# Optimization experiments

Measured on AMD Instinct MI355X. Metric: run time of the kernel, lower is better.

## Reference

```python
import jax, jax.numpy as jnp
import numpy as np

N = 100000       # nodes
E = 1600000      # edges (avg degree 16)
D_IN = 256
D_HID = 64
D_OUT = 40
PROP_STEP = 16
ALP = 0.5
LAM = 1.0


def setup_inputs() -> dict:
    key = jax.random.key(0)
    ks = jax.random.split(key, 9)
    x = jax.random.normal(ks[0], (N, D_IN), dtype=jnp.float32)
    edge_row = jnp.sort(jax.random.randint(ks[1], (E,), 0, N, dtype=jnp.int32))
    edge_col = jax.random.randint(ks[2], (E,), 0, N, dtype=jnp.int32)
    # normalized-adjacency-like nonnegative values, scaled ~1/deg for stability
    edge_val = jax.random.uniform(ks[3], (E,), dtype=jnp.float32) * (1.0 / 16.0)
    diag_vals = jax.random.uniform(ks[4], (N,), dtype=jnp.float32)
    # MLP params (xavier-normal-ish init, zero bias)
    W1 = jax.random.normal(ks[5], (D_IN, D_HID), dtype=jnp.float32) * np.sqrt(2.0 / (D_IN + D_HID))
    b1 = jnp.zeros((D_HID,), dtype=jnp.float32)
    W2 = jax.random.normal(ks[6], (D_HID, D_OUT), dtype=jnp.float32) * np.sqrt(2.0 / (D_HID + D_OUT))
    b2 = jnp.zeros((D_OUT,), dtype=jnp.float32)
    return {"x": x, "edge_row": edge_row, "edge_col": edge_col,
            "edge_val": edge_val, "diag_vals": diag_vals,
            "W1": W1, "b1": b1, "W2": W2, "b2": b2}


def _spmm(edge_row, edge_col, edge_val, Y):
    # sparse [N,N] @ dense [N,D] via gather + segment-sum
    msgs = edge_val[:, None] * Y[edge_col]          # [E, D]
    return jax.ops.segment_sum(msgs, edge_row, num_segments=N)


def reference(x, edge_row, edge_col, edge_val, diag_vals, W1, b1, W2, b2):
    # mlp_bef: single Linear (num_mlp_before=1, no activation after last layer)
    h = x @ W1 + b1                                  # [N, D_HID]
    # spmm(norm_diag, h) is loop-invariant: norm_diag is diagonal
    src = ALP * diag_vals[:, None] * h               # [N, D_HID]
    Y = h
    for _ in range(PROP_STEP):
        Y = (1.0 - ALP) * Y + (ALP * LAM) * _spmm(edge_row, edge_col, edge_val, Y) + src
    # mlp_aft: init_activate=True -> ReLU (norm='none', dropout=0), then Linear
    Y = jax.nn.relu(Y)
    return Y @ W2 + b2                               # [N, D_OUT]
```

## Files before the change

### kernel.cpp

```cpp
#include <hip/hip_runtime.h>

#define N_NODES 100000
#define N_EDGES 1600000
#define D_IN    256
#define D_HID   64
#define D_OUT   40
#define PROP_N  16

typedef short short8 __attribute__((ext_vector_type(8)));
typedef float f32x4  __attribute__((ext_vector_type(4)));

__device__ __forceinline__ unsigned char f32_to_fp8(float f) {
    int p = __builtin_amdgcn_cvt_pk_fp8_f32(f, f, 0, false);
    return (unsigned char)(p & 0xff);
}
__device__ __forceinline__ unsigned short f32_to_bf16(float f) {
    unsigned int u = __float_as_uint(f);
    unsigned int r = (u + 0x7fffu + ((u >> 16) & 1u)) >> 16;
    return (unsigned short)r;
}
__device__ __forceinline__ unsigned int f32x2_to_bf16x2(float lo, float hi) {
    return (unsigned int)f32_to_bf16(lo) | ((unsigned int)f32_to_bf16(hi) << 16);
}
__device__ __forceinline__ float bf16_f(unsigned short u) {
    return __uint_as_float(((unsigned)u) << 16);
}
__device__ __forceinline__ float edge_val(unsigned p) {
    return __uint_as_float((p & 0x7fffu) << 16);
}
__device__ __forceinline__ void fma4(float4& a, float v, unsigned b) {
    a.x = fmaf(v, __builtin_amdgcn_cvt_f32_fp8((int)b, 0), a.x);
    a.y = fmaf(v, __builtin_amdgcn_cvt_f32_fp8((int)b, 1), a.y);
    a.z = fmaf(v, __builtin_amdgcn_cvt_f32_fp8((int)b, 2), a.z);
    a.w = fmaf(v, __builtin_amdgcn_cvt_f32_fp8((int)b, 3), a.w);
}

__global__ __launch_bounds__(256) void build_rowptr(const int* __restrict__ erow,
                                                    int* __restrict__ rp) {
    int r = blockIdx.x * blockDim.x + threadIdx.x;
    if (r > N_NODES) return;
    int lo = 0, hi = N_EDGES;
    while (lo < hi) {
        int mid = (lo + hi) >> 1;
        if (erow[mid] < r) lo = mid + 1; else hi = mid;
    }
    rp[r] = lo;
}

__global__ __launch_bounds__(256) void pack_edges4(const int* __restrict__ ecol,
                                                   const float* __restrict__ evalv,
                                                   unsigned* __restrict__ ep4) {
    int i = blockIdx.x * blockDim.x + threadIdx.x;
    if (i >= N_EDGES) return;
    unsigned bf = f32_to_bf16(evalv[i]);
    ep4[i] = ((unsigned)ecol[i] << 15) | (bf & 0x7fffu);
}

__global__ __launch_bounds__(256) void prep_w1t(const float* __restrict__ W1,
                                                unsigned short* __restrict__ W1T) {
    int i = blockIdx.x * 256 + threadIdx.x;
    if (i >= D_IN * D_HID) return;
    int k = i >> 6, n = i & 63;
    W1T[n * 256 + k] = f32_to_bf16(W1[i]);
}

__global__ __launch_bounds__(64) void mlp1(const float* __restrict__ x,
                                           const unsigned short* __restrict__ W1T,
                                           const float* __restrict__ b1,
                                           const float* __restrict__ diag,
                                           unsigned short* __restrict__ Yb,
                                           unsigned char* __restrict__ Y08,
                                           unsigned short* __restrict__ srcb) {
    const int lane  = threadIdx.x;
    const int l15   = lane & 15;
    const int quad  = lane >> 4;
    const int mbase = blockIdx.x * 16;

    f32x4 acc[4] = {};
    const float* xrow = x + (size_t)(mbase + l15) * D_IN + quad * 8;

    #pragma unroll
    for (int ks = 0; ks < 8; ++ks) {
        float4 f0 = *(const float4*)(xrow + ks * 32);
        float4 f1 = *(const float4*)(xrow + ks * 32 + 4);
        union { short8 v; unsigned int u[4]; } a;
        a.u[0] = f32x2_to_bf16x2(f0.x, f0.y);
        a.u[1] = f32x2_to_bf16x2(f0.z, f0.w);
        a.u[2] = f32x2_to_bf16x2(f1.x, f1.y);
        a.u[3] = f32x2_to_bf16x2(f1.z, f1.w);

        #pragma unroll
        for (int ct = 0; ct < 4; ++ct) {
            short8 b = *(const short8*)(W1T + (ct * 16 + l15) * 256 + ks * 32 + quad * 8);
            acc[ct] = __builtin_amdgcn_mfma_f32_16x16x32_bf16(a.v, b, acc[ct], 0, 0, 0);
        }
    }

    float bias[4];
    #pragma unroll
    for (int ct = 0; ct < 4; ++ct) bias[ct] = b1[ct * 16 + l15];

    #pragma unroll
    for (int reg = 0; reg < 4; ++reg) {
        const int mr = mbase + quad * 4 + reg;
        const float dg = diag[mr];
        #pragma unroll
        for (int ct = 0; ct < 4; ++ct) {
            const int col = ct * 16 + l15;
            const float h = acc[ct][reg] + bias[ct];
            const size_t idx = (size_t)mr * 64 + col;
            Yb[idx]   = f32_to_bf16(h);
            srcb[idx] = f32_to_bf16(0.5f * dg * h);
            Y08[idx]  = f32_to_fp8(h);
        }
    }
}

__global__ __launch_bounds__(256) void prop_step(const unsigned short* __restrict__ Yb,
                                                 const unsigned char* __restrict__ Y8,
                                                 const unsigned short* __restrict__ srcb,
                                                 unsigned short* __restrict__ Ybo,
                                                 unsigned char* __restrict__ Yo8,
                                                 const int* __restrict__ rp,
                                                 const unsigned* __restrict__ ep4) {
    const int wid  = blockIdx.x * 4 + (threadIdx.x >> 6);
    const int lane = threadIdx.x & 63;
    const int g    = lane >> 4;
    const int fl   = lane & 15;
    const int row  = wid * 4 + g;

    const int e0 = rp[row];
    const int e1 = rp[row + 1];

    const size_t fb = (size_t)row * 64 + fl * 4;
    const ushort4 ys4 = *(const ushort4*)(Yb + fb);
    const ushort4 sv4 = *(const ushort4*)(srcb + fb);
    const float4 yself = make_float4(bf16_f(ys4.x), bf16_f(ys4.y),
                                     bf16_f(ys4.z), bf16_f(ys4.w));
    const float4 sv    = make_float4(bf16_f(sv4.x), bf16_f(sv4.y),
                                     bf16_f(sv4.z), bf16_f(sv4.w));
    const unsigned char* Y8f = Y8 + fl * 4;

    float4 acc0 = make_float4(0.f, 0.f, 0.f, 0.f);
    float4 acc1 = acc0, acc2 = acc0, acc3 = acc0;

    int e = e0;
    int ea = (e0 + 3) & ~3;
    if (ea > e1) ea = e1;
    for (; e < ea; ++e) {
        unsigned p = ep4[e];
        unsigned b = *(const unsigned*)(Y8f + ((size_t)(p >> 15) << 6));
        fma4(acc0, edge_val(p), b);
    }
    for (; e + 8 <= e1; e += 8) {
        uint4 pa = *(const uint4*)(ep4 + e);
        uint4 pb = *(const uint4*)(ep4 + e + 4);
        unsigned b0 = *(const unsigned*)(Y8f + ((size_t)(pa.x >> 15) << 6));
        unsigned b1 = *(const unsigned*)(Y8f + ((size_t)(pa.y >> 15) << 6));
        unsigned b2 = *(const unsigned*)(Y8f + ((size_t)(pa.z >> 15) << 6));
        unsigned b3 = *(const unsigned*)(Y8f + ((size_t)(pa.w >> 15) << 6));
        unsigned b4 = *(const unsigned*)(Y8f + ((size_t)(pb.x >> 15) << 6));
        unsigned b5 = *(const unsigned*)(Y8f + ((size_t)(pb.y >> 15) << 6));
        unsigned b6 = *(const unsigned*)(Y8f + ((size_t)(pb.z >> 15) << 6));
        unsigned b7 = *(const unsigned*)(Y8f + ((size_t)(pb.w >> 15) << 6));
        fma4(acc0, edge_val(pa.x), b0);
        fma4(acc1, edge_val(pa.y), b1);
        fma4(acc2, edge_val(pa.z), b2);
        fma4(acc3, edge_val(pa.w), b3);
        fma4(acc0, edge_val(pb.x), b4);
        fma4(acc1, edge_val(pb.y), b5);
        fma4(acc2, edge_val(pb.z), b6);
        fma4(acc3, edge_val(pb.w), b7);
    }
    if (e + 4 <= e1) {
        uint4 pa = *(const uint4*)(ep4 + e);
        unsigned b0 = *(const unsigned*)(Y8f + ((size_t)(pa.x >> 15) << 6));
        unsigned b1 = *(const unsigned*)(Y8f + ((size_t)(pa.y >> 15) << 6));
        unsigned b2 = *(const unsigned*)(Y8f + ((size_t)(pa.z >> 15) << 6));
        unsigned b3 = *(const unsigned*)(Y8f + ((size_t)(pa.w >> 15) << 6));
        fma4(acc0, edge_val(pa.x), b0);
        fma4(acc1, edge_val(pa.y), b1);
        fma4(acc2, edge_val(pa.z), b2);
        fma4(acc3, edge_val(pa.w), b3);
        e += 4;
    }
    for (; e < e1; ++e) {
        unsigned p = ep4[e];
        unsigned b = *(const unsigned*)(Y8f + ((size_t)(p >> 15) << 6));
        fma4(acc0, edge_val(p), b);
    }

    float4 accs;
    accs.x = (acc0.x + acc1.x) + (acc2.x + acc3.x);
    accs.y = (acc0.y + acc1.y) + (acc2.y + acc3.y);
    accs.z = (acc0.z + acc1.z) + (acc2.z + acc3.z);
    accs.w = (acc0.w + acc1.w) + (acc2.w + acc3.w);

    float4 o;
    o.x = fmaf(0.5f, yself.x, fmaf(0.5f, accs.x, sv.x));
    o.y = fmaf(0.5f, yself.y, fmaf(0.5f, accs.y, sv.y));
    o.z = fmaf(0.5f, yself.z, fmaf(0.5f, accs.z, sv.z));
    o.w = fmaf(0.5f, yself.w, fmaf(0.5f, accs.w, sv.w));

    ushort4 ob;
    ob.x = f32_to_bf16(o.x); ob.y = f32_to_bf16(o.y);
    ob.z = f32_to_bf16(o.z); ob.w = f32_to_bf16(o.w);
    *(ushort4*)(Ybo + fb) = ob;
    int pk = __builtin_amdgcn_cvt_pk_fp8_f32(o.x, o.y, 0, false);
    pk     = __builtin_amdgcn_cvt_pk_fp8_f32(o.z, o.w, pk, true);
    *(unsigned*)(Yo8 + fb) = (unsigned)pk;
}

__global__ __launch_bounds__(256) void mlp2(const unsigned short* __restrict__ Yb,
                                            const float* __restrict__ W2,
                                            const float* __restrict__ b2,
                                            float* __restrict__ out) {
    __shared__ float W2s[D_HID * D_OUT];
    __shared__ float b2s[D_OUT];
    int tid = threadIdx.x;
    for (int i = tid; i < D_HID * D_OUT; i += 256) W2s[i] = W2[i];
    if (tid < D_OUT) b2s[tid] = b2[tid];
    __syncthreads();

    int n = blockIdx.x * 256 + tid;
    if (n >= N_NODES) return;

    float acc[D_OUT];
    #pragma unroll
    for (int o = 0; o < D_OUT; ++o) acc[o] = b2s[o];

    const uint4* Y4 = (const uint4*)(Yb + (size_t)n * 64);
    #pragma unroll
    for (int k8 = 0; k8 < 8; ++k8) {
        uint4 y = Y4[k8];
        unsigned w[4] = {y.x, y.y, y.z, y.w};
        #pragma unroll
        for (int d = 0; d < 4; ++d) {
            float lo = fmaxf(__uint_as_float((w[d] & 0xffffu) << 16), 0.0f);
            float hi = fmaxf(__uint_as_float(w[d] & 0xffff0000u), 0.0f);
            int klo = k8 * 8 + 2 * d, khi = klo + 1;
            #pragma unroll
            for (int o = 0; o < D_OUT; ++o)
                acc[o] = fmaf(lo, W2s[klo * D_OUT + o], acc[o]);
            #pragma unroll
            for (int o = 0; o < D_OUT; ++o)
                acc[o] = fmaf(hi, W2s[khi * D_OUT + o], acc[o]);
        }
    }

    float4* o4 = (float4*)(out + (size_t)n * D_OUT);
    #pragma unroll
    for (int q = 0; q < 10; ++q)
        o4[q] = make_float4(acc[4 * q], acc[4 * q + 1], acc[4 * q + 2], acc[4 * q + 3]);
}

extern "C" void kernel_launch(void* const* d_in, const int* in_sizes, int n_in,
                              void* d_out, int out_size, void* d_ws, size_t ws_size,
                              hipStream_t stream) {
    const float* x     = (const float*)d_in[0];
    const int*   erow  = (const int*)  d_in[1];
    const int*   ecol  = (const int*)  d_in[2];
    const float* evalv = (const float*)d_in[3];
    const float* diag  = (const float*)d_in[4];
    const float* W1    = (const float*)d_in[5];
    const float* b1    = (const float*)d_in[6];
    const float* W2    = (const float*)d_in[7];
    const float* b2    = (const float*)d_in[8];
    float* out = (float*)d_out;

    const size_t NV = (size_t)N_NODES * D_HID;
    unsigned short* Yb0  = (unsigned short*)d_ws;
    unsigned short* Yb1  = Yb0 + NV;
    unsigned short* srcb = Yb1 + NV;
    unsigned char*  Y08  = (unsigned char*)(srcb + NV);
    unsigned char*  Y18  = Y08 + NV;
    unsigned*       ep4  = (unsigned*)(Y18 + NV);
    int*            rp   = (int*)(ep4 + N_EDGES);
    unsigned short* W1T  = (unsigned short*)
        (((unsigned long long)(rp + N_NODES + 1) + 15ull) & ~15ull);

    build_rowptr<<<(N_NODES + 1 + 255) / 256, 256, 0, stream>>>(erow, rp);
    pack_edges4<<<(N_EDGES + 255) / 256, 256, 0, stream>>>(ecol, evalv, ep4);
    prep_w1t<<<(D_IN * D_HID + 255) / 256, 256, 0, stream>>>(W1, W1T);
    mlp1<<<N_NODES / 16, 64, 0, stream>>>(x, W1T, b1, diag, Yb0, Y08, srcb);

    unsigned short* Yb[2] = {Yb0, Yb1};
    unsigned char*  Y8[2] = {Y08, Y18};
    for (int i = 0; i < PROP_N; ++i) {
        prop_step<<<N_NODES / 16, 256, 0, stream>>>(
            Yb[i & 1], Y8[i & 1], srcb, Yb[(i + 1) & 1], Y8[(i + 1) & 1], rp, ep4);
    }
    mlp2<<<(N_NODES + 255) / 256, 256, 0, stream>>>(Yb0, W2, b2, out);
}
```

Baseline: 752.0 us.

## Split SpMM gather into two column-range passes for cache locality

Each row's edges are partitioned by source column into two halves, below and above node 50000, and every propagation step becomes two kernel passes, each gathering only from one half of the fp8 feature table. The aim is to keep each pass's gather working set (about 3.2 MB) resident in cache. In exchange it adds an fp32 partial-sum buffer that is written and then read back, doubles the kernel launches, and drops the vectorized uint4 edge loads because partitioned segments are no longer aligned.

```diff
diff --git a/kernel.cpp b/kernel.cpp
--- a/kernel.cpp
+++ b/kernel.cpp
@@ -6,6 +6,7 @@
 #define D_HID   64
 #define D_OUT   40
 #define PROP_N  16
+#define COL_SPLIT 50000u
 
 typedef short short8 __attribute__((ext_vector_type(8)));
 typedef float f32x4  __attribute__((ext_vector_type(4)));
@@ -54,6 +55,24 @@
     if (i >= N_EDGES) return;
     unsigned bf = f32_to_bf16(evalv[i]);
     ep4[i] = ((unsigned)ecol[i] << 15) | (bf & 0x7fffu);
+}
+
+__global__ __launch_bounds__(256) void part_edges(const int* __restrict__ rp,
+                                                  const unsigned* __restrict__ ep4,
+                                                  unsigned* __restrict__ ep2,
+                                                  int* __restrict__ rs) {
+    int r = blockIdx.x * blockDim.x + threadIdx.x;
+    if (r >= N_NODES) return;
+    int e0 = rp[r], e1 = rp[r + 1];
+    int cnt = 0;
+    for (int e = e0; e < e1; ++e) cnt += ((ep4[e] >> 15) < COL_SPLIT);
+    rs[r] = e0 + cnt;
+    int plo = e0, phi = e0 + cnt;
+    for (int e = e0; e < e1; ++e) {
+        unsigned p = ep4[e];
+        if ((p >> 15) < COL_SPLIT) ep2[plo++] = p;
+        else                       ep2[phi++] = p;
+    }
 }
 
 __global__ __launch_bounds__(256) void prep_w1t(const float* __restrict__ W1,
@@ -116,78 +135,68 @@
     }
 }
 
-__global__ __launch_bounds__(256) void prop_step(const unsigned short* __restrict__ Yb,
-                                                 const unsigned char* __restrict__ Y8,
+__global__ __launch_bounds__(256) void prop_pass(const unsigned char* __restrict__ Y8,
+                                                 const unsigned* __restrict__ ep2,
+                                                 const int* __restrict__ bptr,
+                                                 const int* __restrict__ eptr,
+                                                 float* __restrict__ tmp,
+                                                 const unsigned short* __restrict__ Yb,
                                                  const unsigned short* __restrict__ srcb,
                                                  unsigned short* __restrict__ Ybo,
                                                  unsigned char* __restrict__ Yo8,
-                                                 const int* __restrict__ rp,
-                                                 const unsigned* __restrict__ ep4) {
+                                                 const int mode) {
     const int wid  = blockIdx.x * 4 + (threadIdx.x >> 6);
     const int lane = threadIdx.x & 63;
     const int g    = lane >> 4;
     const int fl   = lane & 15;
     const int row  = wid * 4 + g;
 
-    const int e0 = rp[row];
-    const int e1 = rp[row + 1];
+    const int b0 = bptr[row];
+    const int e1 = eptr[row];
 
     const size_t fb = (size_t)row * 64 + fl * 4;
-    const ushort4 ys4 = *(const ushort4*)(Yb + fb);
-    const ushort4 sv4 = *(const ushort4*)(srcb + fb);
-    const float4 yself = make_float4(bf16_f(ys4.x), bf16_f(ys4.y),
-                                     bf16_f(ys4.z), bf16_f(ys4.w));
-    const float4 sv    = make_float4(bf16_f(sv4.x), bf16_f(sv4.y),
-                                     bf16_f(sv4.z), bf16_f(sv4.w));
     const unsigned char* Y8f = Y8 + fl * 4;
 
     float4 acc0 = make_float4(0.f, 0.f, 0.f, 0.f);
     float4 acc1 = acc0, acc2 = acc0, acc3 = acc0;
 
-    int e = e0;
-    int ea = (e0 + 3) & ~3;
-    if (ea > e1) ea = e1;
-    for (; e < ea; ++e) {
-        unsigned p = ep4[e];
-        unsigned b = *(const unsigned*)(Y8f + ((size_t)(p >> 15) << 6));
-        fma4(acc0, edge_val(p), b);
-    }
+    int e = b0;
     for (; e + 8 <= e1; e += 8) {
-        uint4 pa = *(const uint4*)(ep4 + e);
-        uint4 pb = *(const uint4*)(ep4 + e + 4);
-        unsigned b0 = *(const unsigned*)(Y8f + ((size_t)(pa.x >> 15) << 6));
-        unsigned b1 = *(const unsigned*)(Y8f + ((size_t)(pa.y >> 15) << 6));
-        unsigned b2 = *(const unsigned*)(Y8f + ((size_t)(pa.z >> 15) << 6));
-        unsigned b3 = *(const unsigned*)(Y8f + ((size_t)(pa.w >> 15) << 6));
-        unsigned b4 = *(const unsigned*)(Y8f + ((size_t)(pb.x >> 15) << 6));
-        unsigned b5 = *(const unsigned*)(Y8f + ((size_t)(pb.y >> 15) << 6));
-        unsigned b6 = *(const unsigned*)(Y8f + ((size_t)(pb.z >> 15) << 6));
-        unsigned b7 = *(const unsigned*)(Y8f + ((size_t)(pb.w >> 15) << 6));
-        fma4(acc0, edge_val(pa.x), b0);
-        fma4(acc1, edge_val(pa.y), b1);
-        fma4(acc2, edge_val(pa.z), b2);
-        fma4(acc3, edge_val(pa.w), b3);
-        fma4(acc0, edge_val(pb.x), b4);
-        fma4(acc1, edge_val(pb.y), b5);
-        fma4(acc2, edge_val(pb.z), b6);
-        fma4(acc3, edge_val(pb.w), b7);
+        unsigned p0 = ep2[e + 0], p1 = ep2[e + 1], p2 = ep2[e + 2], p3 = ep2[e + 3];
+        unsigned p4 = ep2[e + 4], p5 = ep2[e + 5], p6 = ep2[e + 6], p7 = ep2[e + 7];
+        unsigned q0 = *(const unsigned*)(Y8f + ((size_t)(p0 >> 15) << 6));
+        unsigned q1 = *(const unsigned*)(Y8f + ((size_t)(p1 >> 15) << 6));
+        unsigned q2 = *(const unsigned*)(Y8f + ((size_t)(p2 >> 15) << 6));
+        unsigned q3 = *(const unsigned*)(Y8f + ((size_t)(p3 >> 15) << 6));
+        unsigned q4 = *(const unsigned*)(Y8f + ((size_t)(p4 >> 15) << 6));
+        unsigned q5 = *(const unsigned*)(Y8f + ((size_t)(p5 >> 15) << 6));
+        unsigned q6 = *(const unsigned*)(Y8f + ((size_t)(p6 >> 15) << 6));
+        unsigned q7 = *(const unsigned*)(Y8f + ((size_t)(p7 >> 15) << 6));
+        fma4(acc0, edge_val(p0), q0);
+        fma4(acc1, edge_val(p1), q1);
+        fma4(acc2, edge_val(p2), q2);
+        fma4(acc3, edge_val(p3), q3);
+        fma4(acc0, edge_val(p4), q4);
+        fma4(acc1, edge_val(p5), q5);
+        fma4(acc2, edge_val(p6), q6);
+        fma4(acc3, edge_val(p7), q7);
     }
     if (e + 4 <= e1) {
-        uint4 pa = *(const uint4*)(ep4 + e);
-        unsigned b0 = *(const unsigned*)(Y8f + ((size_t)(pa.x >> 15) << 6));
-        unsigned b1 = *(const unsigned*)(Y8f + ((size_t)(pa.y >> 15) << 6));
-        unsigned b2 = *(const unsigned*)(Y8f + ((size_t)(pa.z >> 15) << 6));
-        unsigned b3 = *(const unsigned*)(Y8f + ((size_t)(pa.w >> 15) << 6));
-        fma4(acc0, edge_val(pa.x), b0);
-        fma4(acc1, edge_val(pa.y), b1);
-        fma4(acc2, edge_val(pa.z), b2);
-        fma4(acc3, edge_val(pa.w), b3);
+        unsigned p0 = ep2[e + 0], p1 = ep2[e + 1], p2 = ep2[e + 2], p3 = ep2[e + 3];
+        unsigned q0 = *(const unsigned*)(Y8f + ((size_t)(p0 >> 15) << 6));
+        unsigned q1 = *(const unsigned*)(Y8f + ((size_t)(p1 >> 15) << 6));
+        unsigned q2 = *(const unsigned*)(Y8f + ((size_t)(p2 >> 15) << 6));
+        unsigned q3 = *(const unsigned*)(Y8f + ((size_t)(p3 >> 15) << 6));
+        fma4(acc0, edge_val(p0), q0);
+        fma4(acc1, edge_val(p1), q1);
+        fma4(acc2, edge_val(p2), q2);
+        fma4(acc3, edge_val(p3), q3);
         e += 4;
     }
     for (; e < e1; ++e) {
-        unsigned p = ep4[e];
-        unsigned b = *(const unsigned*)(Y8f + ((size_t)(p >> 15) << 6));
-        fma4(acc0, edge_val(p), b);
+        unsigned p = ep2[e];
+        unsigned q = *(const unsigned*)(Y8f + ((size_t)(p >> 15) << 6));
+        fma4(acc0, edge_val(p), q);
     }
 
     float4 accs;
@@ -196,11 +205,22 @@
     accs.z = (acc0.z + acc1.z) + (acc2.z + acc3.z);
     accs.w = (acc0.w + acc1.w) + (acc2.w + acc3.w);
 
+    if (mode == 0) {
+        *(float4*)(tmp + fb) = accs;
+        return;
+    }
+
+    const float4 t = *(const float4*)(tmp + fb);
+    accs.x += t.x; accs.y += t.y; accs.z += t.z; accs.w += t.w;
+
+    const ushort4 ys4 = *(const ushort4*)(Yb + fb);
+    const ushort4 sv4 = *(const ushort4*)(srcb + fb);
+
     float4 o;
-    o.x = fmaf(0.5f, yself.x, fmaf(0.5f, accs.x, sv.x));
-    o.y = fmaf(0.5f, yself.y, fmaf(0.5f, accs.y, sv.y));
-    o.z = fmaf(0.5f, yself.z, fmaf(0.5f, accs.z, sv.z));
-    o.w = fmaf(0.5f, yself.w, fmaf(0.5f, accs.w, sv.w));
+    o.x = fmaf(0.5f, bf16_f(ys4.x), fmaf(0.5f, accs.x, bf16_f(sv4.x)));
+    o.y = fmaf(0.5f, bf16_f(ys4.y), fmaf(0.5f, accs.y, bf16_f(sv4.y)));
+    o.z = fmaf(0.5f, bf16_f(ys4.z), fmaf(0.5f, accs.z, bf16_f(sv4.z)));
+    o.w = fmaf(0.5f, bf16_f(ys4.w), fmaf(0.5f, accs.w, bf16_f(sv4.w)));
 
     ushort4 ob;
     ob.x = f32_to_bf16(o.x); ob.y = f32_to_bf16(o.y);
@@ -274,21 +294,28 @@
     unsigned short* srcb = Yb1 + NV;
     unsigned char*  Y08  = (unsigned char*)(srcb + NV);
     unsigned char*  Y18  = Y08 + NV;
-    unsigned*       ep4  = (unsigned*)(Y18 + NV);
-    int*            rp   = (int*)(ep4 + N_EDGES);
+    float*          tmp  = (float*)(Y18 + NV);
+    unsigned*       ep4  = (unsigned*)(tmp + NV);
+    unsigned*       ep2  = ep4 + N_EDGES;
+    int*            rp   = (int*)(ep2 + N_EDGES);
+    int*            rs   = rp + (N_NODES + 1);
     unsigned short* W1T  = (unsigned short*)
-        (((unsigned long long)(rp + N_NODES + 1) + 15ull) & ~15ull);
+        (((unsigned long long)(rs + N_NODES) + 15ull) & ~15ull);
 
     build_rowptr<<<(N_NODES + 1 + 255) / 256, 256, 0, stream>>>(erow, rp);
     pack_edges4<<<(N_EDGES + 255) / 256, 256, 0, stream>>>(ecol, evalv, ep4);
+    part_edges<<<(N_NODES + 255) / 256, 256, 0, stream>>>(rp, ep4, ep2, rs);
     prep_w1t<<<(D_IN * D_HID + 255) / 256, 256, 0, stream>>>(W1, W1T);
     mlp1<<<N_NODES / 16, 64, 0, stream>>>(x, W1T, b1, diag, Yb0, Y08, srcb);
 
     unsigned short* Yb[2] = {Yb0, Yb1};
     unsigned char*  Y8[2] = {Y08, Y18};
     for (int i = 0; i < PROP_N; ++i) {
-        prop_step<<<N_NODES / 16, 256, 0, stream>>>(
-            Yb[i & 1], Y8[i & 1], srcb, Yb[(i + 1) & 1], Y8[(i + 1) & 1], rp, ep4);
+        const int c = i & 1, n = (i + 1) & 1;
+        prop_pass<<<N_NODES / 16, 256, 0, stream>>>(
+            Y8[c], ep2, rp, rs, tmp, nullptr, nullptr, nullptr, nullptr, 0);
+        prop_pass<<<N_NODES / 16, 256, 0, stream>>>(
+            Y8[c], ep2, rs, rp + 1, tmp, Yb[c], srcb, Yb[n], Y8[n], 1);
     }
     mlp2<<<(N_NODES + 255) / 256, 256, 0, stream>>>(Yb0, W2, b2, out);
 }
```

Measured after the change: 927.5 us. 23.3% more time.
